# Kernel optimization log

Measured on AMD Instinct MI355X. Metric: run time of the kernel, lower is better.

The kernel has to match this reference:

```python
import jax, jax.numpy as jnp
import numpy as np

C = 256
CQK = C // 8


def setup_inputs() -> dict:
    key = jax.random.key(0)
    ks = jax.random.split(key, 8)
    B, H, W = 4, 64, 64
    x = jax.random.normal(ks[0], (B, C, H, W), dtype=jnp.float32)
    # 1x1 conv weights are plain [out_c, in_c] matrices + bias
    sq = 1.0 / np.sqrt(C)
    Wq = jax.random.uniform(ks[1], (CQK, C), jnp.float32, -sq, sq)
    bq = jax.random.uniform(ks[2], (CQK,), jnp.float32, -sq, sq)
    Wk = jax.random.uniform(ks[3], (CQK, C), jnp.float32, -sq, sq)
    bk = jax.random.uniform(ks[4], (CQK,), jnp.float32, -sq, sq)
    Wv = jax.random.uniform(ks[5], (C, C), jnp.float32, -sq, sq)
    bv = jax.random.uniform(ks[6], (C,), jnp.float32, -sq, sq)
    gamma = jnp.zeros((1,), dtype=jnp.float32)
    return {"x": x, "Wq": Wq, "bq": bq, "Wk": Wk, "bk": bk, "Wv": Wv, "bv": bv, "gamma": gamma}


def reference(x, Wq, bq, Wk, bk, Wv, bv, gamma):
    B, Cc, H, W = x.shape
    N = H * W
    xf = x.reshape(B, Cc, N)  # [B, C, N]
    # 1x1 convs == channel GEMMs
    q = jnp.einsum('dc,bcn->bdn', Wq, xf) + bq[None, :, None]  # [B, C/8, N]
    k = jnp.einsum('dc,bcn->bdn', Wk, xf) + bk[None, :, None]  # [B, C/8, N]
    v = jnp.einsum('dc,bcn->bdn', Wv, xf) + bv[None, :, None]  # [B, C, N]
    # attention[b, i, j] = softmax_j( q_i . k_j )  (no scaling, as in source)
    attn = jax.nn.softmax(jnp.einsum('bdn,bdm->bnm', q, k), axis=-1)  # [B, N, N]
    # out = value @ attention  (note: NOT attention^T, faithful to source)
    out = jnp.einsum('bcn,bnm->bcm', v, attn)  # [B, C, N]
    out = out.reshape(B, Cc, H, W)
    return gamma[0] * out + x
```

## Files before the change

### kernel.cpp

```cpp
#include <hip/hip_runtime.h>
#include <hip/hip_bf16.h>


#define NB 4
#define CC 256
#define NN 4096
#define L2E 1.44269504088896340f

typedef short  short4v  __attribute__((ext_vector_type(4)));
typedef short  short8v  __attribute__((ext_vector_type(8)));
typedef __bf16 bf16x8   __attribute__((ext_vector_type(8)));
typedef float  f32x4    __attribute__((ext_vector_type(4)));
typedef float  f32x16   __attribute__((ext_vector_type(16)));
typedef unsigned long u64x2 __attribute__((ext_vector_type(2)));
typedef unsigned int u32;

static __device__ __forceinline__ unsigned short f2bf(float f) {
  union { __bf16 h; unsigned short u; } v; v.h = (__bf16)f; return v.u;
}
static __device__ __forceinline__ float bf2f(unsigned short u) {
  union { unsigned u; float f; } v; v.u = (u32)u << 16; return v.f;
}

union FragU { short8v s; bf16x8 b; unsigned u[4]; };

static __device__ __forceinline__ bf16x8 ld_frag(const unsigned short* p) {
  FragU u; u.s = *(const short8v*)p; return u.b;
}

static __device__ __forceinline__ f32x16 zero16() {
  f32x16 v;
#pragma unroll
  for (int i = 0; i < 16; ++i) v[i] = 0.0f;
  return v;
}

static __device__ __forceinline__ f32x16 mfma32(bf16x8 a, bf16x8 b, f32x16 c) {
  return __builtin_amdgcn_mfma_f32_32x32x16_bf16(a, b, c, 0, 0, 0);
}
static __device__ __forceinline__ f32x16 mfma8(long a, long b, f32x16 c) {
  return __builtin_amdgcn_mfma_f32_32x32x16_fp8_fp8(a, b, c, 0, 0, 0);
}

__global__ __launch_bounds__(256) void k_wcvt(
    const float* __restrict__ Wq, const float* __restrict__ Wk,
    const float* __restrict__ Wv, unsigned short* __restrict__ Wb)
{
  const int i4 = blockIdx.x * 256 + threadIdx.x;
  const int e = i4 * 4;
  const int row = e >> 8, c = e & 255;
  const float* src = (row < 32) ? (Wq + row * 256 + c)
                   : (row < 64) ? (Wk + (row - 32) * 256 + c)
                                : (Wv + (row - 64) * 256 + c);
  f32x4 v = *(const f32x4*)src;
  short4v s;
#pragma unroll
  for (int j = 0; j < 4; ++j) s[j] = (short)f2bf(v[j]);
  *(short4v*)(Wb + e) = s;
}

__global__ __launch_bounds__(256) void k_proj(
    const float* __restrict__ x, const unsigned short* __restrict__ Wb,
    const float* __restrict__ bq, const float* __restrict__ bk,
    const float* __restrict__ bv,
    unsigned short* __restrict__ Qt, unsigned short* __restrict__ Kt,
    unsigned char* __restrict__ V8)
{
  __shared__ unsigned short xs[32][268];
  const int t = threadIdx.x;
  const int b = blockIdx.y;
  const int n0 = blockIdx.x * 32;
  const int w = t >> 6, l = t & 63, h = l >> 5, col = l & 31;

  const float* xb = x + (size_t)b * CC * NN;
  {
    const int c_off = t >> 3, nl = 4 * (t & 7);
#pragma unroll
    for (int c0 = 0; c0 < CC; c0 += 32) {
      int c = c0 + c_off;
      f32x4 v4 = *(const f32x4*)(xb + (size_t)c * NN + n0 + nl);
#pragma unroll
      for (int j = 0; j < 4; ++j) xs[nl + j][c] = f2bf(v4[j]);
    }
  }
  __syncthreads();

  for (int f = w; f < 10; f += 4) {
    const float* bsrc; int rowbase; int mode; int wrow;
    if (f == 0)      { bsrc = bq; rowbase = 0;            mode = 0; wrow = 0; }
    else if (f == 1) { bsrc = bk; rowbase = 0;            mode = 1; wrow = 32; }
    else             { bsrc = bv; rowbase = (f - 2) * 32; mode = 2; wrow = 64 + rowbase; }

    f32x16 acc0 = zero16();
    const unsigned short* wr = Wb + (size_t)(wrow + col) * 256 + 8 * h;

#pragma unroll
    for (int k0 = 0; k0 < CC; k0 += 16) {
      FragU a;
      a.s = *(const short8v*)(wr + k0);
      const unsigned short* p0 = &xs[col][k0 + 8 * h];
      FragU b0;
      short4v t0a = *(const short4v*)p0, t0b = *(const short4v*)(p0 + 4);
#pragma unroll
      for (int j = 0; j < 4; ++j) { b0.s[j] = t0a[j]; b0.s[4 + j] = t0b[j]; }
      acc0 = mfma32(a.b, b0.b, acc0);
    }

    const int n = n0 + col;
#pragma unroll
    for (int q = 0; q < 4; ++q) {
      f32x4 bias4 = *(const f32x4*)(bsrc + rowbase + 8 * q + 4 * h);
      float vals[4];
#pragma unroll
      for (int i = 0; i < 4; ++i) vals[i] = acc0[4 * q + i] + bias4[i];
      if (mode == 2) {
        const size_t tb = ((((size_t)b * 128 + (n >> 5)) * 2 + ((n >> 3) & 1)) * 256) * 16
                          + ((n >> 4) & 1) * 8 + (n & 7);
        u32 w01 = __builtin_amdgcn_cvt_pk_fp8_f32(vals[0], vals[1], 0, false);
        u32 w23 = __builtin_amdgcn_cvt_pk_fp8_f32(vals[2], vals[3], 0, false);
        const int cb0 = rowbase + 8 * q + 4 * h;
        V8[tb + (size_t)(cb0 + 0) * 16] = (unsigned char)(w01 & 0xff);
        V8[tb + (size_t)(cb0 + 1) * 16] = (unsigned char)((w01 >> 8) & 0xff);
        V8[tb + (size_t)(cb0 + 2) * 16] = (unsigned char)(w23 & 0xff);
        V8[tb + (size_t)(cb0 + 3) * 16] = (unsigned char)((w23 >> 8) & 0xff);
      } else {
        unsigned short* dst = (mode == 0) ? Qt : Kt;
        const float scale = (mode == 0) ? L2E : 1.0f;
        short4v s4;
#pragma unroll
        for (int i = 0; i < 4; ++i) s4[i] = (short)f2bf(vals[i] * scale);
        *(short4v*)(dst + ((size_t)b * NN + n) * 32 + 8 * q + 4 * h) = s4;
      }
    }
  }
}

__global__ __launch_bounds__(512) void k_rowstats(
    const unsigned short* __restrict__ Qt, const unsigned short* __restrict__ Kt,
    float* __restrict__ cbias)
{
  __shared__ float ssum[8][64];
  const int t = threadIdx.x;
  const int w = t >> 6, l = t & 63, h = l >> 5, col = l & 31;
  const int b = blockIdx.y;
  const int n0 = blockIdx.x * 64;
  const unsigned short* Qb = Qt + (size_t)b * NN * 32;
  const unsigned short* Kb = Kt + (size_t)b * NN * 32;

  bf16x8 bq00 = ld_frag(Qb + (size_t)(n0 + col) * 32 + 8 * h);
  bf16x8 bq01 = ld_frag(Qb + (size_t)(n0 + col) * 32 + 16 + 8 * h);
  bf16x8 bq10 = ld_frag(Qb + (size_t)(n0 + 32 + col) * 32 + 8 * h);
  bf16x8 bq11 = ld_frag(Qb + (size_t)(n0 + 32 + col) * 32 + 16 + 8 * h);

  float acc0 = 0.0f, acc1 = 0.0f;
  const int mbase = w * (NN / 8);
#pragma unroll 2
  for (int mt = 0; mt < 16; ++mt) {
    const int m0 = mbase + mt * 32;
    bf16x8 ak0 = ld_frag(Kb + (size_t)(m0 + col) * 32 + 8 * h);
    bf16x8 ak1 = ld_frag(Kb + (size_t)(m0 + col) * 32 + 16 + 8 * h);
    f32x16 S0 = zero16(), S1 = zero16();
    S0 = mfma32(ak0, bq00, S0);
    S0 = mfma32(ak1, bq01, S0);
    S1 = mfma32(ak0, bq10, S1);
    S1 = mfma32(ak1, bq11, S1);
    float p0 = 0.0f, p1 = 0.0f, p2 = 0.0f, p3 = 0.0f;
#pragma unroll
    for (int r = 0; r < 8; ++r) {
      p0 += __builtin_amdgcn_exp2f(S0[r]);
      p1 += __builtin_amdgcn_exp2f(S0[8 + r]);
      p2 += __builtin_amdgcn_exp2f(S1[r]);
      p3 += __builtin_amdgcn_exp2f(S1[8 + r]);
    }
    acc0 += p0 + p1;
    acc1 += p2 + p3;
  }
  acc0 += __shfl_xor(acc0, 32);
  acc1 += __shfl_xor(acc1, 32);

  if (l < 32) { ssum[w][l] = acc0; ssum[w][32 + l] = acc1; }
  __syncthreads();

  if (t < 64) {
    float s = 0.0f;
#pragma unroll
    for (int wv = 0; wv < 8; ++wv) s += ssum[wv][t];
    cbias[(size_t)b * NN + n0 + t] = -__builtin_amdgcn_logf(s);
  }
}

__global__ __launch_bounds__(512) void k_emat(
    const unsigned short* __restrict__ Qt, const unsigned short* __restrict__ Kt,
    const float* __restrict__ cbias, unsigned char* __restrict__ E8)
{
  const int t = threadIdx.x;
  const int w = t >> 6, l = t & 63, h = l >> 5, col = l & 31;
  const int b = blockIdx.y;
  const int n0 = blockIdx.x * 32;
  const unsigned short* Qb = Qt + (size_t)b * NN * 32;
  const unsigned short* Kb = Kt + (size_t)b * NN * 32;

  bf16x8 aq0 = ld_frag(Qb + (size_t)(n0 + col) * 32 + 8 * h);
  bf16x8 aq1 = ld_frag(Qb + (size_t)(n0 + col) * 32 + 16 + 8 * h);

  f32x4 cb4[4];
  const float* cbi = cbias + (size_t)b * NN + n0;
#pragma unroll
  for (int q = 0; q < 4; ++q) cb4[q] = *(const f32x4*)(cbi + 8 * q + 4 * h);

  unsigned char* st = E8 + ((size_t)b * 512 + 2 * (size_t)(n0 >> 4) + h) * 32768;

#pragma unroll 2
  for (int mt = 0; mt < 16; ++mt) {
    const int m0 = w * 512 + mt * 32;
    bf16x8 bk0 = ld_frag(Kb + (size_t)(m0 + col) * 32 + 8 * h);
    bf16x8 bk1 = ld_frag(Kb + (size_t)(m0 + col) * 32 + 16 + 8 * h);
    f32x16 S = zero16();
    S = mfma32(aq0, bk0, S);
    S = mfma32(aq1, bk1, S);

    float e[16];
#pragma unroll
    for (int q = 0; q < 4; ++q)
#pragma unroll
      for (int i = 0; i < 4; ++i)
        e[4 * q + i] = __builtin_amdgcn_exp2f(S[4 * q + i] + cb4[q][i]);

    u32 wA = __builtin_amdgcn_cvt_pk_fp8_f32(e[0], e[1], 0, false);
    wA = __builtin_amdgcn_cvt_pk_fp8_f32(e[2], e[3], wA, true);
    u32 wB = __builtin_amdgcn_cvt_pk_fp8_f32(e[4], e[5], 0, false);
    wB = __builtin_amdgcn_cvt_pk_fp8_f32(e[6], e[7], wB, true);
    u32 wC = __builtin_amdgcn_cvt_pk_fp8_f32(e[8], e[9], 0, false);
    wC = __builtin_amdgcn_cvt_pk_fp8_f32(e[10], e[11], wC, true);
    u32 wD = __builtin_amdgcn_cvt_pk_fp8_f32(e[12], e[13], 0, false);
    wD = __builtin_amdgcn_cvt_pk_fp8_f32(e[14], e[15], wD, true);
    asm("v_permlane32_swap_b32 %0, %1" : "+v"(wA), "+v"(wB));
    asm("v_permlane32_swap_b32 %0, %1" : "+v"(wC), "+v"(wD));
    unsigned long ev0 = ((unsigned long)wB << 32) | wA;
    unsigned long ev1 = ((unsigned long)wD << 32) | wC;

    *(unsigned long*)(st + (size_t)(m0 + col) * 8) = ev0;
    *(unsigned long*)(st + 65536 + (size_t)(m0 + col) * 8) = ev1;
  }
}

__global__ __launch_bounds__(256) void k_pv(
    const unsigned char* __restrict__ E8, const unsigned char* __restrict__ V8,
    const float* __restrict__ x, const float* __restrict__ gamma,
    float* __restrict__ out)
{
  __shared__ unsigned short ldb[32][264];
  const int t = threadIdx.x;
  const int w = t >> 6, l = t & 63, h = l >> 5, col = l & 31;
  const int b = blockIdx.y;
  const int m0 = blockIdx.x * 32;
  const int cc = w * 64;

  const unsigned char* ep = E8 + ((size_t)b * 512 + h) * 32768
                            + (size_t)(m0 + col) * 8;
  const unsigned char* vp = V8 + ((size_t)b * 256 + h) * 4096
                            + (size_t)(cc + col) * 16;

  f32x16 acc[2];
  acc[0] = zero16();
  acc[1] = zero16();

  unsigned long e0c = *(const unsigned long*)(ep);
  unsigned long e1c = *(const unsigned long*)(ep + 65536);
  u64x2 vAc = *(const u64x2*)(vp);
  u64x2 vBc = *(const u64x2*)(vp + 512);
  ep += 131072; vp += 8192;

#pragma unroll 4
  for (int nt = 0; nt < 127; ++nt) {
    unsigned long e0n = *(const unsigned long*)(ep);
    unsigned long e1n = *(const unsigned long*)(ep + 65536);
    u64x2 vAn = *(const u64x2*)(vp);
    u64x2 vBn = *(const u64x2*)(vp + 512);
    ep += 131072; vp += 8192;
    acc[0] = mfma8((long)e0c, (long)vAc[0], acc[0]);
    acc[1] = mfma8((long)e0c, (long)vBc[0], acc[1]);
    acc[0] = mfma8((long)e1c, (long)vAc[1], acc[0]);
    acc[1] = mfma8((long)e1c, (long)vBc[1], acc[1]);
    e0c = e0n; e1c = e1n; vAc = vAn; vBc = vBn;
  }
  acc[0] = mfma8((long)e0c, (long)vAc[0], acc[0]);
  acc[1] = mfma8((long)e0c, (long)vBc[0], acc[1]);
  acc[0] = mfma8((long)e1c, (long)vAc[1], acc[0]);
  acc[1] = mfma8((long)e1c, (long)vBc[1], acc[1]);

#pragma unroll
  for (int cf = 0; cf < 2; ++cf)
#pragma unroll
    for (int r = 0; r < 16; ++r) {
      int mloc = (r & 3) + 8 * (r >> 2) + 4 * h;
      ldb[mloc][cc + 32 * cf + col] = f2bf(acc[cf][r]);
    }
  __syncthreads();

  const float g = gamma[0];
  const int ci = t >> 3;
  const int m4 = (t & 7) * 4;
#pragma unroll
  for (int rnd = 0; rnd < 8; ++rnd) {
    const int c = 32 * rnd + ci;
    const size_t idx = ((size_t)b * CC + c) * NN + m0 + m4;
    f32x4 xv = *(const f32x4*)(x + idx);
    f32x4 o;
#pragma unroll
    for (int k = 0; k < 4; ++k) o[k] = g * bf2f(ldb[m4 + k][c]) + xv[k];
    *(f32x4*)(out + idx) = o;
  }
}

extern "C" void kernel_launch(void* const* d_in, const int* in_sizes, int n_in,
                              void* d_out, int out_size, void* d_ws, size_t ws_size,
                              hipStream_t stream) {
  const float* x     = (const float*)d_in[0];
  const float* Wq    = (const float*)d_in[1];
  const float* bq    = (const float*)d_in[2];
  const float* Wk    = (const float*)d_in[3];
  const float* bk    = (const float*)d_in[4];
  const float* Wv    = (const float*)d_in[5];
  const float* bv    = (const float*)d_in[6];
  const float* gamma = (const float*)d_in[7];
  float* out = (float*)d_out;

  char* ws = (char*)d_ws;
  unsigned short* Qt = (unsigned short*)(ws);
  unsigned short* Kt = (unsigned short*)(ws + (1u << 20));
  unsigned char*  V8 = (unsigned char*)(ws + (2u << 20));
  unsigned short* Wb = (unsigned short*)(ws + (6u << 20));
  float* cbias = (float*)(ws + (6u << 20) + (1u << 18));
  unsigned char* E8  = (unsigned char*)(ws + (7u << 20));

  k_wcvt<<<dim3(80), 256, 0, stream>>>(Wq, Wk, Wv, Wb);
  k_proj<<<dim3(NN / 32, NB), 256, 0, stream>>>(x, Wb, bq, bk, bv, Qt, Kt, V8);
  k_rowstats<<<dim3(NN / 64, NB), 512, 0, stream>>>(Qt, Kt, cbias);
  k_emat<<<dim3(NN / 32, NB), 512, 0, stream>>>(Qt, Kt, cbias, E8);
  k_pv<<<dim3(NN / 32, NB), 256, 0, stream>>>(E8, V8, x, gamma, out);
}
```

Baseline: 100.7 us.

## Re-tile fp8 attention-weight buffer for contiguous PV reads and deepen prefetch

The QK/exp kernel now writes the fp8 attention weights in a layout grouped by PV output block, one 128 KB chunk per 32-column block. Each PV block then walks its own contiguous region in 1 KB steps instead of striding 128 KB per iteration, which should improve DRAM/TLB locality. The PV loop also switches from a one-stage to a four-stage register prefetch to hide more load latency. The final prefetch iterations read past each block's chunk, and past the end of the buffer for the last block; those values are never used.

```diff
diff --git a/kernel.cpp b/kernel.cpp
--- a/kernel.cpp
+++ b/kernel.cpp
@@ -14,6 +14,7 @@
 typedef float  f32x16   __attribute__((ext_vector_type(16)));
 typedef unsigned long u64x2 __attribute__((ext_vector_type(2)));
 typedef unsigned int u32;
+typedef unsigned long u64;
 
 static __device__ __forceinline__ unsigned short f2bf(float f) {
   union { __bf16 h; unsigned short u; } v; v.h = (__bf16)f; return v.u;
@@ -208,7 +209,7 @@
 #pragma unroll
   for (int q = 0; q < 4; ++q) cb4[q] = *(const f32x4*)(cbi + 8 * q + 4 * h);
 
-  unsigned char* st = E8 + ((size_t)b * 512 + 2 * (size_t)(n0 >> 4) + h) * 32768;
+  const size_t gh_off = (size_t)(n0 >> 5) * 1024 + (size_t)h * 256 + (size_t)col * 8;
 
 #pragma unroll 2
   for (int mt = 0; mt < 16; ++mt) {
@@ -236,11 +237,12 @@
     wD = __builtin_amdgcn_cvt_pk_fp8_f32(e[14], e[15], wD, true);
     asm("v_permlane32_swap_b32 %0, %1" : "+v"(wA), "+v"(wB));
     asm("v_permlane32_swap_b32 %0, %1" : "+v"(wC), "+v"(wD));
-    unsigned long ev0 = ((unsigned long)wB << 32) | wA;
-    unsigned long ev1 = ((unsigned long)wD << 32) | wC;
-
-    *(unsigned long*)(st + (size_t)(m0 + col) * 8) = ev0;
-    *(unsigned long*)(st + 65536 + (size_t)(m0 + col) * 8) = ev1;
+    u64 ev0 = ((u64)wB << 32) | wA;
+    u64 ev1 = ((u64)wD << 32) | wC;
+
+    unsigned char* st = E8 + ((size_t)b * 128 + (size_t)(w * 16 + mt)) * 131072 + gh_off;
+    *(u64*)(st) = ev0;
+    *(u64*)(st + 512) = ev1;
   }
 }
 
@@ -256,8 +258,8 @@
   const int m0 = blockIdx.x * 32;
   const int cc = w * 64;
 
-  const unsigned char* ep = E8 + ((size_t)b * 512 + h) * 32768
-                            + (size_t)(m0 + col) * 8;
+  const unsigned char* ep = E8 + ((size_t)b * 128 + blockIdx.x) * 131072
+                            + (size_t)h * 256 + (size_t)col * 8;
   const unsigned char* vp = V8 + ((size_t)b * 256 + h) * 4096
                             + (size_t)(cc + col) * 16;
 
@@ -265,29 +267,31 @@
   acc[0] = zero16();
   acc[1] = zero16();
 
-  unsigned long e0c = *(const unsigned long*)(ep);
-  unsigned long e1c = *(const unsigned long*)(ep + 65536);
-  u64x2 vAc = *(const u64x2*)(vp);
-  u64x2 vBc = *(const u64x2*)(vp + 512);
-  ep += 131072; vp += 8192;
-
-#pragma unroll 4
-  for (int nt = 0; nt < 127; ++nt) {
-    unsigned long e0n = *(const unsigned long*)(ep);
-    unsigned long e1n = *(const unsigned long*)(ep + 65536);
-    u64x2 vAn = *(const u64x2*)(vp);
-    u64x2 vBn = *(const u64x2*)(vp + 512);
-    ep += 131072; vp += 8192;
-    acc[0] = mfma8((long)e0c, (long)vAc[0], acc[0]);
-    acc[1] = mfma8((long)e0c, (long)vBc[0], acc[1]);
-    acc[0] = mfma8((long)e1c, (long)vAc[1], acc[0]);
-    acc[1] = mfma8((long)e1c, (long)vBc[1], acc[1]);
-    e0c = e0n; e1c = e1n; vAc = vAn; vBc = vBn;
-  }
-  acc[0] = mfma8((long)e0c, (long)vAc[0], acc[0]);
-  acc[1] = mfma8((long)e0c, (long)vBc[0], acc[1]);
-  acc[0] = mfma8((long)e1c, (long)vAc[1], acc[0]);
-  acc[1] = mfma8((long)e1c, (long)vBc[1], acc[1]);
+  u64 e0p[4], e1p[4];
+  u64x2 vAp[4], vBp[4];
+#pragma unroll
+  for (int s = 0; s < 4; ++s) {
+    e0p[s] = *(const u64*)(ep + (size_t)s * 1024);
+    e1p[s] = *(const u64*)(ep + (size_t)s * 1024 + 512);
+    vAp[s] = *(const u64x2*)(vp + (size_t)s * 8192);
+    vBp[s] = *(const u64x2*)(vp + (size_t)s * 8192 + 512);
+  }
+
+  for (int gg = 0; gg < 128; gg += 4) {
+#pragma unroll
+    for (int s = 0; s < 4; ++s) {
+      const int gn = gg + 4 + s;
+      u64 ne0 = *(const u64*)(ep + (size_t)gn * 1024);
+      u64 ne1 = *(const u64*)(ep + (size_t)gn * 1024 + 512);
+      u64x2 nvA = *(const u64x2*)(vp + (size_t)gn * 8192);
+      u64x2 nvB = *(const u64x2*)(vp + (size_t)gn * 8192 + 512);
+      acc[0] = mfma8((long)e0p[s], (long)vAp[s][0], acc[0]);
+      acc[1] = mfma8((long)e0p[s], (long)vBp[s][0], acc[1]);
+      acc[0] = mfma8((long)e1p[s], (long)vAp[s][1], acc[0]);
+      acc[1] = mfma8((long)e1p[s], (long)vBp[s][1], acc[1]);
+      e0p[s] = ne0; e1p[s] = ne1; vAp[s] = nvA; vBp[s] = nvB;
+    }
+  }
 
 #pragma unroll
   for (int cf = 0; cf < 2; ++cf)
```

Result: faster. 94.42 us (-6.2%).
